# Kernel optimization log

Measured on AMD Instinct MI355X. Metric: run time of the kernel, lower is better.

The kernel has to match this reference:

```python
import jax, jax.numpy as jnp
import numpy as np

N = 50000
DIM = 768   # input_dim == feature dim (self.L)
D_ATT = 128 # self.D


def setup_inputs() -> dict:
    key = jax.random.key(0)
    ks = jax.random.split(key, 6)
    s = lambda fan_in: 1.0 / np.sqrt(fan_in)
    return {
        "x": jax.random.normal(ks[0], (1, N, DIM), dtype=jnp.float32),
        "W_feat": jax.random.normal(ks[1], (DIM, DIM), dtype=jnp.float32) * s(DIM),
        "b_feat": jax.random.normal(ks[2], (DIM,), dtype=jnp.float32) * s(DIM),
        "W_a": jax.random.normal(ks[3], (D_ATT, DIM), dtype=jnp.float32) * s(DIM),
        "W_b": jax.random.normal(ks[4], (D_ATT, DIM), dtype=jnp.float32) * s(DIM),
        "W_c": jax.random.normal(ks[5], (1, D_ATT), dtype=jnp.float32) * s(D_ATT),
    }


def reference(x, W_feat, b_feat, W_a, W_b, W_c):
    # x: [1, N, DIM] -> squeeze bag dim -> [N, DIM]
    h = jax.nn.relu(jnp.einsum('nd,ed->ne', x[0], W_feat) + b_feat)  # [N, 768]
    a = jax.nn.relu(jnp.einsum('nd,kd->nk', h, W_a))      # [N, 128]
    b = jax.nn.sigmoid(jnp.einsum('nd,kd->nk', h, W_b))   # [N, 128]
    logits = jnp.einsum('nk,ok->on', a * b, W_c)           # [1, N] (transpose fused)
    A = jax.nn.softmax(logits, axis=-1)                    # [1, N]
    return jnp.einsum('on,nd->od', A, h)                   # [1, 768]
```

## Files before the change

kernel.cpp:

```cpp
#include <hip/hip_runtime.h>
#include <hip/hip_bf16.h>
#include <stdint.h>

#define DEVINL __device__ __forceinline__

using bf16x8 = __attribute__((ext_vector_type(8))) short;
using f32x4  = __attribute__((ext_vector_type(4))) float;

static constexpr int NPTS = 50000;
static constexpr int NPAD = 50048;
static constexpr int DIM  = 768;
static constexpr int DATT = 128;
static constexpr int NRB  = NPAD / 128;

DEVINL ushort f2b(float f) {
  uint32_t u = __float_as_uint(f);
  u += 0x7fffu + ((u >> 16) & 1u);
  return (ushort)(u >> 16);
}
DEVINL float b2f(ushort u) { return __uint_as_float(((uint32_t)u) << 16); }

DEVINL void gload_lds16(const void* g, void* l) {
  __builtin_amdgcn_global_load_lds((const __attribute__((address_space(1))) void*)g,
                                   (__attribute__((address_space(3))) void*)l,
                                   16, 0, 0);
}

__global__ void cvt8_kernel(const float* __restrict__ src, ushort* __restrict__ dst,
                            int n8_src, int n8_dst) {
  const int stride = gridDim.x * blockDim.x;
  for (int i = blockIdx.x * blockDim.x + threadIdx.x; i < n8_dst; i += stride) {
    float4 v0 = {0.f, 0.f, 0.f, 0.f}, v1 = {0.f, 0.f, 0.f, 0.f};
    if (i < n8_src) {
      const float4* s4 = (const float4*)src;
      v0 = s4[(long)i * 2];
      v1 = s4[(long)i * 2 + 1];
    }
    ushort4 o0 = { f2b(v0.x), f2b(v0.y), f2b(v0.z), f2b(v0.w) };
    ushort4 o1 = { f2b(v1.x), f2b(v1.y), f2b(v1.z), f2b(v1.w) };
    ((ushort4*)dst)[(long)i * 2]     = o0;
    ((ushort4*)dst)[(long)i * 2 + 1] = o1;
  }
}

__global__ __launch_bounds__(256)
void gemm_h_kernel(const ushort* __restrict__ A, const ushort* __restrict__ B,
                   const float* __restrict__ bias, ushort* __restrict__ H) {
  __shared__ ushort As[128 * 64];
  __shared__ ushort Bs[128 * 64];
  const int tid  = threadIdx.x;
  const int wid  = tid >> 6;
  const int lane = tid & 63;
  const int col0 = blockIdx.x * 128;
  const int row0 = blockIdx.y * 128;

  const int wr = (wid >> 1) * 64;
  const int wc = (wid & 1) * 64;

  f32x4 acc[4][4] = {};

  const int ld_r = lane >> 3;
  const int ld_c = (lane & 7) * 8;

  for (int k0 = 0; k0 < DIM; k0 += 64) {
    __syncthreads();
#pragma unroll
    for (int i = 0; i < 4; ++i) {
      const int ch = i * 4 + wid;
      const int r  = ch * 8 + ld_r;
      gload_lds16(A + (long)(row0 + r) * DIM + k0 + ld_c, As + ch * 512);
      gload_lds16(B + (long)(col0 + r) * DIM + k0 + ld_c, Bs + ch * 512);
    }
    __syncthreads();
#pragma unroll
    for (int kk = 0; kk < 2; ++kk) {
      const int kc = kk * 32 + (lane >> 4) * 8;
      bf16x8 a[4];
#pragma unroll
      for (int m = 0; m < 4; ++m)
        a[m] = *(const bf16x8*)(As + (wr + m * 16 + (lane & 15)) * 64 + kc);
#pragma unroll
      for (int n = 0; n < 4; ++n) {
        bf16x8 b = *(const bf16x8*)(Bs + (wc + n * 16 + (lane & 15)) * 64 + kc);
#pragma unroll
        for (int m = 0; m < 4; ++m)
          acc[m][n] = __builtin_amdgcn_mfma_f32_16x16x32_bf16(a[m], b, acc[m][n], 0, 0, 0);
      }
    }
  }

  const int lq = lane >> 4;
  const int lc = lane & 15;
#pragma unroll
  for (int n = 0; n < 4; ++n) {
    const int cg = col0 + wc + n * 16 + lc;
    const float bv = bias[cg];
#pragma unroll
    for (int m = 0; m < 4; ++m) {
      const int rg = row0 + wr + m * 16 + lq * 4;
#pragma unroll
      for (int r = 0; r < 4; ++r) {
        float v = acc[m][n][r] + bv;
        v = fmaxf(v, 0.0f);
        H[(long)(rg + r) * DIM + cg] = f2b(v);
      }
    }
  }
}

__global__ __launch_bounds__(512)
void gate_kernel(const ushort* __restrict__ Hm, const ushort* __restrict__ Wa,
                 const ushort* __restrict__ Wb, const float* __restrict__ Wc,
                 float* __restrict__ logits) {
  __shared__ ushort Hs [128 * 64];
  __shared__ ushort Was[128 * 64];
  __shared__ ushort Wbs[128 * 64];
  const int tid  = threadIdx.x;
  const int wid  = tid >> 6;
  const int lane = tid & 63;
  const int row0 = blockIdx.x * 128;

  f32x4 fa[8] = {};
  f32x4 fb[8] = {};

  const int ld_r = lane >> 3;
  const int ld_c = (lane & 7) * 8;

  for (int k0 = 0; k0 < DIM; k0 += 64) {
    __syncthreads();
#pragma unroll
    for (int i = 0; i < 2; ++i) {
      const int ch = i * 8 + wid;
      const int r  = ch * 8 + ld_r;
      gload_lds16(Hm + (long)(row0 + r) * DIM + k0 + ld_c, Hs  + ch * 512);
      gload_lds16(Wa + (long)r * DIM        + k0 + ld_c, Was + ch * 512);
      gload_lds16(Wb + (long)r * DIM        + k0 + ld_c, Wbs + ch * 512);
    }
    __syncthreads();
#pragma unroll
    for (int kk = 0; kk < 2; ++kk) {
      const int kc = kk * 32 + (lane >> 4) * 8;
      bf16x8 h = *(const bf16x8*)(Hs + (wid * 16 + (lane & 15)) * 64 + kc);
#pragma unroll
      for (int n = 0; n < 8; ++n) {
        bf16x8 wa = *(const bf16x8*)(Was + (n * 16 + (lane & 15)) * 64 + kc);
        bf16x8 wb = *(const bf16x8*)(Wbs + (n * 16 + (lane & 15)) * 64 + kc);
        fa[n] = __builtin_amdgcn_mfma_f32_16x16x32_bf16(h, wa, fa[n], 0, 0, 0);
        fb[n] = __builtin_amdgcn_mfma_f32_16x16x32_bf16(h, wb, fb[n], 0, 0, 0);
      }
    }
  }

  const int lc = lane & 15;
  const int lq = lane >> 4;
  float g[4];
#pragma unroll
  for (int r = 0; r < 4; ++r) {
    float s = 0.f;
#pragma unroll
    for (int n = 0; n < 8; ++n) {
      float av = fmaxf(fa[n][r], 0.f);
      float sg = 1.f / (1.f + expf(-fb[n][r]));
      s += av * sg * Wc[n * 16 + lc];
    }
    s += __shfl_xor(s, 1);
    s += __shfl_xor(s, 2);
    s += __shfl_xor(s, 4);
    s += __shfl_xor(s, 8);
    g[r] = s;
  }
  if (lc == 0) {
    const int rbase = row0 + wid * 16 + lq * 4;
#pragma unroll
    for (int r = 0; r < 4; ++r) {
      const int nidx = rbase + r;
      if (nidx < NPTS) logits[nidx] = g[r];
    }
  }
}

__global__ __launch_bounds__(1024)
void softmax_stats_kernel(const float* __restrict__ logits, float* __restrict__ stats) {
  __shared__ float red[1024];
  const int tid = threadIdx.x;
  float m = -1e30f;
  for (int i = tid; i < NPTS; i += 1024) m = fmaxf(m, logits[i]);
  red[tid] = m; __syncthreads();
  for (int s = 512; s > 0; s >>= 1) {
    if (tid < s) red[tid] = fmaxf(red[tid], red[tid + s]);
    __syncthreads();
  }
  m = red[0];
  __syncthreads();
  float sum = 0.f;
  for (int i = tid; i < NPTS; i += 1024) sum += expf(logits[i] - m);
  red[tid] = sum; __syncthreads();
  for (int s = 512; s > 0; s >>= 1) {
    if (tid < s) red[tid] += red[tid + s];
    __syncthreads();
  }
  if (tid == 0) { stats[0] = m; stats[1] = red[0]; }
}

__global__ __launch_bounds__(192)
void weighted_partial_kernel(const ushort* __restrict__ Hm, const float* __restrict__ logits,
                             const float* __restrict__ stats, float* __restrict__ part) {
  __shared__ float w[128];
  const int b = blockIdx.x, tid = threadIdx.x;
  const int n0 = b * 128;
  if (tid < 128) {
    const int n = n0 + tid;
    w[tid] = (n < NPTS) ? expf(logits[n] - stats[0]) : 0.f;
  }
  __syncthreads();
  float4 acc = {0.f, 0.f, 0.f, 0.f};
  const ushort* hp = Hm + (long)n0 * DIM + tid * 4;
#pragma unroll 4
  for (int r = 0; r < 128; ++r) {
    const float wr = w[r];
    ushort4 v = *(const ushort4*)(hp + (long)r * DIM);
    acc.x += wr * b2f(v.x);
    acc.y += wr * b2f(v.y);
    acc.z += wr * b2f(v.z);
    acc.w += wr * b2f(v.w);
  }
  ((float4*)(part + (long)b * DIM))[tid] = acc;
}

__global__ void final_reduce_kernel(const float* __restrict__ part,
                                    const float* __restrict__ stats,
                                    float* __restrict__ out) {
  const int c = blockIdx.x * blockDim.x + threadIdx.x;
  if (c >= DIM) return;
  float s = 0.f;
  for (int b = 0; b < NRB; ++b) s += part[(long)b * DIM + c];
  out[c] = s / stats[1];
}

extern "C" void kernel_launch(void* const* d_in, const int* in_sizes, int n_in,
                              void* d_out, int out_size, void* d_ws, size_t ws_size,
                              hipStream_t stream) {
  const float* x  = (const float*)d_in[0];
  const float* Wf = (const float*)d_in[1];
  const float* bf = (const float*)d_in[2];
  const float* Wa = (const float*)d_in[3];
  const float* Wb = (const float*)d_in[4];
  const float* Wc = (const float*)d_in[5];
  float* out = (float*)d_out;

  char* p = (char*)d_ws;
  ushort* xb  = (ushort*)p; p += (size_t)NPAD * DIM * 2;
  ushort* hb  = (ushort*)p; p += (size_t)NPAD * DIM * 2;
  ushort* wfb = (ushort*)p; p += (size_t)DIM * DIM * 2;
  ushort* wab = (ushort*)p; p += (size_t)DATT * DIM * 2;
  ushort* wbb = (ushort*)p; p += (size_t)DATT * DIM * 2;
  float* logits = (float*)p; p += (size_t)NPAD * 4;
  float* stats  = (float*)p; p += 256;
  float* part   = (float*)p; p += (size_t)NRB * DIM * 4;

  cvt8_kernel<<<2048, 256, 0, stream>>>(x,  xb,  NPTS * DIM / 8, NPAD * DIM / 8);
  cvt8_kernel<<<288,  256, 0, stream>>>(Wf, wfb, DIM * DIM / 8,  DIM * DIM / 8);
  cvt8_kernel<<<48,   256, 0, stream>>>(Wa, wab, DATT * DIM / 8, DATT * DIM / 8);
  cvt8_kernel<<<48,   256, 0, stream>>>(Wb, wbb, DATT * DIM / 8, DATT * DIM / 8);

  gemm_h_kernel<<<dim3(6, NRB), 256, 0, stream>>>(xb, wfb, bf, hb);
  gate_kernel<<<NRB, 512, 0, stream>>>(hb, wab, wbb, Wc, logits);
  softmax_stats_kernel<<<1, 1024, 0, stream>>>(logits, stats);
  weighted_partial_kernel<<<NRB, 192, 0, stream>>>(hb, logits, stats, part);
  final_reduce_kernel<<<3, 256, 0, stream>>>(part, stats, out);
}
```

Before: 248.1 us.

## Widen feature GEMM tile to 128x256, remap blocks per XCD, merge weight casts

The H GEMM now uses 512-thread blocks that compute 128x256 output tiles, so each A tile loaded into LDS is reused across twice as many columns. A block-id remap groups consecutive work-groups onto the same XCD, so blocks sharing A rows sit near the same L2. The three weight-conversion launches are merged into one kernel to cut launch overhead. The larger tile raises LDS use per block and lowers the total block count, which may reduce occupancy.

```diff
diff --git a/kernel.cpp b/kernel.cpp
--- a/kernel.cpp
+++ b/kernel.cpp
@@ -43,19 +43,44 @@
   }
 }
 
-__global__ __launch_bounds__(256)
+__global__ void cvt_weights_kernel(const float* __restrict__ Wf, const float* __restrict__ Wa,
+                                   const float* __restrict__ Wb,
+                                   ushort* __restrict__ wfb, ushort* __restrict__ wab,
+                                   ushort* __restrict__ wbb) {
+  const int NF = DIM * DIM / 8, NA = DATT * DIM / 8;
+  int i = blockIdx.x * blockDim.x + threadIdx.x;
+  const float* src; ushort* dst; int j;
+  if (i < NF)               { src = Wf; dst = wfb; j = i; }
+  else if (i < NF + NA)     { src = Wa; dst = wab; j = i - NF; }
+  else if (i < NF + 2 * NA) { src = Wb; dst = wbb; j = i - NF - NA; }
+  else return;
+  const float4* s4 = (const float4*)src;
+  float4 v0 = s4[(long)j * 2];
+  float4 v1 = s4[(long)j * 2 + 1];
+  ushort4 o0 = { f2b(v0.x), f2b(v0.y), f2b(v0.z), f2b(v0.w) };
+  ushort4 o1 = { f2b(v1.x), f2b(v1.y), f2b(v1.z), f2b(v1.w) };
+  ((ushort4*)dst)[(long)j * 2]     = o0;
+  ((ushort4*)dst)[(long)j * 2 + 1] = o1;
+}
+
+__global__ __launch_bounds__(512)
 void gemm_h_kernel(const ushort* __restrict__ A, const ushort* __restrict__ B,
                    const float* __restrict__ bias, ushort* __restrict__ H) {
   __shared__ ushort As[128 * 64];
-  __shared__ ushort Bs[128 * 64];
+  __shared__ ushort Bs[256 * 64];
   const int tid  = threadIdx.x;
   const int wid  = tid >> 6;
   const int lane = tid & 63;
-  const int col0 = blockIdx.x * 128;
-  const int row0 = blockIdx.y * 128;
-
-  const int wr = (wid >> 1) * 64;
-  const int wc = (wid & 1) * 64;
+
+  const int nwg = NRB * 3;
+  const int q = nwg >> 3, r = nwg & 7;
+  const int xcd = blockIdx.x & 7, idx = blockIdx.x >> 3;
+  const int wgid = (xcd < r ? xcd * (q + 1) : r * (q + 1) + (xcd - r) * q) + idx;
+  const int row0 = (wgid / 3) * 128;
+  const int col0 = (wgid % 3) * 256;
+
+  const int wrow = (wid >> 2) * 64;
+  const int wcol = (wid & 3) * 64;
 
   f32x4 acc[4][4] = {};
 
@@ -65,11 +90,14 @@
   for (int k0 = 0; k0 < DIM; k0 += 64) {
     __syncthreads();
 #pragma unroll
+    for (int i = 0; i < 2; ++i) {
+      const int ch = i * 8 + wid;
+      gload_lds16(A + (long)(row0 + ch * 8 + ld_r) * DIM + k0 + ld_c, As + ch * 512);
+    }
+#pragma unroll
     for (int i = 0; i < 4; ++i) {
-      const int ch = i * 4 + wid;
-      const int r  = ch * 8 + ld_r;
-      gload_lds16(A + (long)(row0 + r) * DIM + k0 + ld_c, As + ch * 512);
-      gload_lds16(B + (long)(col0 + r) * DIM + k0 + ld_c, Bs + ch * 512);
+      const int ch = i * 8 + wid;
+      gload_lds16(B + (long)(col0 + ch * 8 + ld_r) * DIM + k0 + ld_c, Bs + ch * 512);
     }
     __syncthreads();
 #pragma unroll
@@ -78,10 +106,10 @@
       bf16x8 a[4];
 #pragma unroll
       for (int m = 0; m < 4; ++m)
-        a[m] = *(const bf16x8*)(As + (wr + m * 16 + (lane & 15)) * 64 + kc);
+        a[m] = *(const bf16x8*)(As + (wrow + m * 16 + (lane & 15)) * 64 + kc);
 #pragma unroll
       for (int n = 0; n < 4; ++n) {
-        bf16x8 b = *(const bf16x8*)(Bs + (wc + n * 16 + (lane & 15)) * 64 + kc);
+        bf16x8 b = *(const bf16x8*)(Bs + (wcol + n * 16 + (lane & 15)) * 64 + kc);
 #pragma unroll
         for (int m = 0; m < 4; ++m)
           acc[m][n] = __builtin_amdgcn_mfma_f32_16x16x32_bf16(a[m], b, acc[m][n], 0, 0, 0);
@@ -93,16 +121,16 @@
   const int lc = lane & 15;
 #pragma unroll
   for (int n = 0; n < 4; ++n) {
-    const int cg = col0 + wc + n * 16 + lc;
+    const int cg = col0 + wcol + n * 16 + lc;
     const float bv = bias[cg];
 #pragma unroll
     for (int m = 0; m < 4; ++m) {
-      const int rg = row0 + wr + m * 16 + lq * 4;
-#pragma unroll
-      for (int r = 0; r < 4; ++r) {
-        float v = acc[m][n][r] + bv;
+      const int rg = row0 + wrow + m * 16 + lq * 4;
+#pragma unroll
+      for (int r2 = 0; r2 < 4; ++r2) {
+        float v = acc[m][n][r2] + bv;
         v = fmaxf(v, 0.0f);
-        H[(long)(rg + r) * DIM + cg] = f2b(v);
+        H[(long)(rg + r2) * DIM + cg] = f2b(v);
       }
     }
   }
@@ -258,12 +286,10 @@
   float* stats  = (float*)p; p += 256;
   float* part   = (float*)p; p += (size_t)NRB * DIM * 4;
 
-  cvt8_kernel<<<2048, 256, 0, stream>>>(x,  xb,  NPTS * DIM / 8, NPAD * DIM / 8);
-  cvt8_kernel<<<288,  256, 0, stream>>>(Wf, wfb, DIM * DIM / 8,  DIM * DIM / 8);
-  cvt8_kernel<<<48,   256, 0, stream>>>(Wa, wab, DATT * DIM / 8, DATT * DIM / 8);
-  cvt8_kernel<<<48,   256, 0, stream>>>(Wb, wbb, DATT * DIM / 8, DATT * DIM / 8);
-
-  gemm_h_kernel<<<dim3(6, NRB), 256, 0, stream>>>(xb, wfb, bf, hb);
+  cvt8_kernel<<<2048, 256, 0, stream>>>(x, xb, NPTS * DIM / 8, NPAD * DIM / 8);
+  cvt_weights_kernel<<<384, 256, 0, stream>>>(Wf, Wa, Wb, wfb, wab, wbb);
+
+  gemm_h_kernel<<<NRB * 3, 512, 0, stream>>>(xb, wfb, bf, hb);
   gate_kernel<<<NRB, 512, 0, stream>>>(hb, wab, wbb, Wc, logits);
   softmax_stats_kernel<<<1, 1024, 0, stream>>>(logits, stats);
   weighted_partial_kernel<<<NRB, 192, 0, stream>>>(hb, logits, stats, part);
```

Measured after the change: 234.3 us. 5.6% less time.
